# Kernel tuning notes

Measured on AMD Instinct MI355X. Metric: run time of the kernel, lower is better.

## Reference

```python
import jax, jax.numpy as jnp
import numpy as np
from jax import lax

THRESHOLD = 0.8
EPS = 1e-3


def _conv2d_same(x, w, b):
    # x: [B,H,W,Cin], w: [3,3,Cin,Cout], b: [Cout]
    y = lax.conv_general_dilated(x, w, window_strides=(1, 1), padding='SAME',
                                 dimension_numbers=('NHWC', 'HWIO', 'NHWC'))
    return y + b


def _region_moments(x, flag):
    # x: [B,H,W,C], flag: [B,H,W,1] in {0,1}
    flag_sum = jnp.sum(jnp.sign(flag), axis=(1, 2), keepdims=True) + EPS
    mu = jnp.sum(x * flag, axis=(1, 2), keepdims=True) / flag_sum
    sigma = jnp.sum((x - mu) ** 2 * flag, axis=(1, 2), keepdims=True) / flag_sum
    return mu, sigma


def setup_inputs() -> dict:
    key = jax.random.key(0)
    k = jax.random.split(key, 4)
    B, H, W, C = 8, 256, 256, 128
    inputs = jax.random.normal(k[0], (B, H, W, C), dtype=jnp.float32)
    w_sr = jax.random.normal(k[1], (3, 3, 2, 1), dtype=jnp.float32) * 0.3
    w_gamma = jax.random.normal(k[2], (3, 3, 1, 1), dtype=jnp.float32) * 0.3
    w_beta = jax.random.normal(k[3], (3, 3, 1, 1), dtype=jnp.float32) * 0.3
    return {
        'inputs': inputs,
        'w_sr': w_sr, 'b_sr': jnp.zeros((1,), jnp.float32),
        'w_gamma': w_gamma, 'b_gamma': jnp.zeros((1,), jnp.float32),
        'w_beta': w_beta, 'b_beta': jnp.zeros((1,), jnp.float32),
    }


def reference(inputs, w_sr, b_sr, w_gamma, b_gamma, w_beta, b_beta):
    maxpool = jnp.max(inputs, axis=-1, keepdims=True)
    avgpool = jnp.mean(inputs, axis=-1, keepdims=True)
    x = jnp.concatenate([maxpool, avgpool], axis=-1)  # [B,H,W,2]
    x = jax.nn.sigmoid(_conv2d_same(x, w_sr, b_sr))   # [B,H,W,1]
    region_mask = jnp.sign(jax.nn.relu(x - THRESHOLD))  # {0,1}

    beta = _conv2d_same(x, w_beta, b_beta)
    gamma = _conv2d_same(x, w_gamma, b_gamma)

    mu_v, sig_v = _region_moments(inputs, region_mask)
    x_valid = (inputs - mu_v) / jnp.sqrt(sig_v + EPS) * region_mask

    inv_mask = 1.0 - region_mask
    mu_m, sig_m = _region_moments(inputs, inv_mask)
    x_mask = (inputs - mu_m) / jnp.sqrt(sig_m + EPS) * inv_mask

    out = x_valid + x_mask
    return out * beta + gamma
```

## Files before the change

kernel.cpp:

```cpp
#include <hip/hip_runtime.h>

#define BB 8
#define HH 256
#define WW 256
#define CC 128
#define HW (HH*WW)
#define NP (BB*HW)
#define THRESHOLD 0.8f
#define EPSV 1e-3f

__global__ __launch_bounds__(256) void k_pool(const float* __restrict__ in,
                                              float2* __restrict__ pooled,
                                              float* __restrict__ zbuf) {
    if (blockIdx.x == 0) {
        for (int i = threadIdx.x; i < 4104; i += 256) zbuf[i] = 0.0f;
    }
    int p    = blockIdx.x * 4 + (threadIdx.x >> 6);
    int lane = threadIdx.x & 63;
    const float2 v = *reinterpret_cast<const float2*>(in + (size_t)p * CC + lane * 2);
    float mx = fmaxf(v.x, v.y);
    float sm = v.x + v.y;
#pragma unroll
    for (int m = 32; m >= 1; m >>= 1) {
        mx = fmaxf(mx, __shfl_xor(mx, m));
        sm += __shfl_xor(sm, m);
    }
    if (lane == 0) pooled[p] = make_float2(mx, sm * (1.0f / 128.0f));
}

__global__ __launch_bounds__(256) void k_mask(const float2* __restrict__ pooled,
                                              const float* __restrict__ w_sr,
                                              const float* __restrict__ b_sr,
                                              const float* __restrict__ w_gamma,
                                              const float* __restrict__ b_gamma,
                                              const float* __restrict__ w_beta,
                                              const float* __restrict__ b_beta,
                                              float* __restrict__ mask,
                                              float2* __restrict__ bg,
                                              float* __restrict__ cnt) {
    int b    = blockIdx.x >> 6;
    int tile = blockIdx.x & 63;
    int th0  = (tile >> 3) * 32;
    int tw0  = (tile & 7) * 32;
    __shared__ float xs[34][35];
    __shared__ float csh;
    if (threadIdx.x == 0) csh = 0.0f;

    float wsr[18], wg[9], wb[9];
#pragma unroll
    for (int i = 0; i < 18; ++i) wsr[i] = w_sr[i];
#pragma unroll
    for (int i = 0; i < 9; ++i) { wg[i] = w_gamma[i]; wb[i] = w_beta[i]; }
    float bsr = b_sr[0], bg0 = b_gamma[0], bb0 = b_beta[0];

    for (int i = threadIdx.x; i < 34 * 34; i += 256) {
        int ly = i / 34, lx = i - ly * 34;
        int h = th0 + ly - 1, w = tw0 + lx - 1;
        float val = 0.0f;
        if ((unsigned)h < HH && (unsigned)w < WW) {
            float acc = bsr;
#pragma unroll
            for (int kh = 0; kh < 3; ++kh) {
                int hh = h + kh - 1;
                if ((unsigned)hh >= HH) continue;
#pragma unroll
                for (int kw = 0; kw < 3; ++kw) {
                    int ww = w + kw - 1;
                    if ((unsigned)ww >= WW) continue;
                    float2 pv = pooled[(size_t)b * HW + hh * WW + ww];
                    acc += pv.x * wsr[(kh * 3 + kw) * 2 + 0] + pv.y * wsr[(kh * 3 + kw) * 2 + 1];
                }
            }
            val = 1.0f / (1.0f + expf(-acc));
        }
        xs[ly][lx] = val;
    }
    __syncthreads();

    float csum = 0.0f;
    for (int i = threadIdx.x; i < 1024; i += 256) {
        int ty = i >> 5, tx = i & 31;
        float xc = xs[ty + 1][tx + 1];
        float m = (xc > THRESHOLD) ? 1.0f : 0.0f;
        csum += m;
        float ag = bg0, ab = bb0;
#pragma unroll
        for (int kh = 0; kh < 3; ++kh)
#pragma unroll
            for (int kw = 0; kw < 3; ++kw) {
                float xv = xs[ty + kh][tx + kw];
                ag += xv * wg[kh * 3 + kw];
                ab += xv * wb[kh * 3 + kw];
            }
        size_t p = (size_t)b * HW + (size_t)(th0 + ty) * WW + (tw0 + tx);
        mask[p] = m;
        bg[p] = make_float2(ab, ag);
    }
    atomicAdd(&csh, csum);
    __syncthreads();
    if (threadIdx.x == 0) atomicAdd(&cnt[b], csh);
}

__global__ __launch_bounds__(256) void k_moments(const float* __restrict__ in,
                                                 const float* __restrict__ mask,
                                                 float* __restrict__ acc) {
    int b     = blockIdx.x >> 7;
    int chunk = blockIdx.x & 127;
    int c4    = threadIdx.x & 31;
    int pg    = threadIdx.x >> 5;
    float4 sv = make_float4(0, 0, 0, 0), ssv = sv, sm = sv, ssm = sv;
    int pbase = chunk * 512;
    for (int i = 0; i < 64; ++i) {
        int pl = pbase + i * 8 + pg;
        size_t p = (size_t)b * HW + pl;
        float m = mask[p];
        const float4 v = *reinterpret_cast<const float4*>(in + p * CC + c4 * 4);
        float4 v2 = make_float4(v.x * v.x, v.y * v.y, v.z * v.z, v.w * v.w);
        if (m > 0.5f) {
            sv.x += v.x; sv.y += v.y; sv.z += v.z; sv.w += v.w;
            ssv.x += v2.x; ssv.y += v2.y; ssv.z += v2.z; ssv.w += v2.w;
        } else {
            sm.x += v.x; sm.y += v.y; sm.z += v.z; sm.w += v.w;
            ssm.x += v2.x; ssm.y += v2.y; ssm.z += v2.z; ssm.w += v2.w;
        }
    }
    __shared__ float4 sh[4][8][32];
    sh[0][pg][c4] = sv; sh[1][pg][c4] = ssv; sh[2][pg][c4] = sm; sh[3][pg][c4] = ssm;
    __syncthreads();
    int t = threadIdx.x;
    if (t < 128) {
        int arr = t >> 5, c = t & 31;
        float4 s = sh[arr][0][c];
#pragma unroll
        for (int j = 1; j < 8; ++j) {
            float4 u = sh[arr][j][c];
            s.x += u.x; s.y += u.y; s.z += u.z; s.w += u.w;
        }
        float* dst = acc + arr * 1024 + b * 128 + c * 4;
        atomicAdd(dst + 0, s.x);
        atomicAdd(dst + 1, s.y);
        atomicAdd(dst + 2, s.z);
        atomicAdd(dst + 3, s.w);
    }
}

__global__ void k_stats(const float* __restrict__ acc, const float* __restrict__ cnt,
                        float* __restrict__ stats) {
    int i = blockIdx.x * 256 + threadIdx.x;
    if (i >= 1024) return;
    int b = i >> 7;
    float cv = cnt[b];
    float cm = (float)HW - cv;
    float s_v = acc[i], ss_v = acc[1024 + i], s_m = acc[2048 + i], ss_m = acc[3072 + i];
    float fs_v = cv + EPSV;
    float mu_v = s_v / fs_v;
    float sig_v = (ss_v - 2.f * mu_v * s_v + mu_v * mu_v * cv) / fs_v;
    float fs_m = cm + EPSV;
    float mu_m = s_m / fs_m;
    float sig_m = (ss_m - 2.f * mu_m * s_m + mu_m * mu_m * cm) / fs_m;
    stats[i]        = mu_v;
    stats[1024 + i] = 1.0f / sqrtf(sig_v + EPSV);
    stats[2048 + i] = mu_m;
    stats[3072 + i] = 1.0f / sqrtf(sig_m + EPSV);
}

__global__ __launch_bounds__(256) void k_apply(const float* __restrict__ in,
                                               const float* __restrict__ mask,
                                               const float2* __restrict__ bg,
                                               const float* __restrict__ stats,
                                               float* __restrict__ out) {
    size_t idx = (size_t)blockIdx.x * 256 + threadIdx.x;
    size_t p = idx >> 5;
    int c4 = (int)(idx & 31);
    int b = (int)(p >> 16);
    const float4 v = reinterpret_cast<const float4*>(in)[idx];
    float m   = mask[p];
    float2 bgv = bg[p];
    float be = bgv.x, ga = bgv.y;
    int off = (m > 0.5f) ? 0 : 2048;
    int si = off + b * 128 + c4 * 4;
    const float4 mu = *reinterpret_cast<const float4*>(stats + si);
    const float4 rs = *reinterpret_cast<const float4*>(stats + si + 1024);
    float4 o;
    o.x = (v.x - mu.x) * rs.x * be + ga;
    o.y = (v.y - mu.y) * rs.y * be + ga;
    o.z = (v.z - mu.z) * rs.z * be + ga;
    o.w = (v.w - mu.w) * rs.w * be + ga;
    reinterpret_cast<float4*>(out)[idx] = o;
}

extern "C" void kernel_launch(void* const* d_in, const int* in_sizes, int n_in,
                              void* d_out, int out_size, void* d_ws, size_t ws_size,
                              hipStream_t stream) {
    const float* in      = (const float*)d_in[0];
    const float* w_sr    = (const float*)d_in[1];
    const float* b_sr    = (const float*)d_in[2];
    const float* w_gamma = (const float*)d_in[3];
    const float* b_gamma = (const float*)d_in[4];
    const float* w_beta  = (const float*)d_in[5];
    const float* b_beta  = (const float*)d_in[6];
    float* out = (float*)d_out;
    float* ws  = (float*)d_ws;

    float2* pooled = (float2*)ws;
    float*  mask   = ws + 2 * (size_t)NP;
    float2* bg     = (float2*)(ws + 3 * (size_t)NP);
    float*  acc    = ws + 5 * (size_t)NP;
    float*  cnt    = acc + 4096;
    float*  stats  = cnt + 8;

    k_pool   <<<NP / 4,  256, 0, stream>>>(in, pooled, acc);
    k_mask   <<<BB * 64, 256, 0, stream>>>(pooled, w_sr, b_sr, w_gamma, b_gamma,
                                           w_beta, b_beta, mask, bg, cnt);
    k_moments<<<BB * 128, 256, 0, stream>>>(in, mask, acc);
    k_stats  <<<4, 256, 0, stream>>>(acc, cnt, stats);
    k_apply  <<<(int)((size_t)NP * CC / 4 / 256), 256, 0, stream>>>(in, mask, bg, stats, out);
}
```

Measured before the change: 580.8 us.

## Fuse total moments into pooling pass and accumulate only minority mask region

New measurement: 552.3 us. -4.9%, faster.

```diff
diff --git a/kernel.cpp b/kernel.cpp
--- a/kernel.cpp
+++ b/kernel.cpp
@@ -11,21 +11,49 @@
 
 __global__ __launch_bounds__(256) void k_pool(const float* __restrict__ in,
                                               float2* __restrict__ pooled,
-                                              float* __restrict__ zbuf) {
-    if (blockIdx.x == 0) {
-        for (int i = threadIdx.x; i < 4104; i += 256) zbuf[i] = 0.0f;
-    }
-    int p    = blockIdx.x * 4 + (threadIdx.x >> 6);
-    int lane = threadIdx.x & 63;
-    const float2 v = *reinterpret_cast<const float2*>(in + (size_t)p * CC + lane * 2);
-    float mx = fmaxf(v.x, v.y);
-    float sm = v.x + v.y;
-#pragma unroll
-    for (int m = 32; m >= 1; m >>= 1) {
-        mx = fmaxf(mx, __shfl_xor(mx, m));
-        sm += __shfl_xor(sm, m);
-    }
-    if (lane == 0) pooled[p] = make_float2(mx, sm * (1.0f / 128.0f));
+                                              float* __restrict__ accT,
+                                              float* __restrict__ accTS) {
+    int b     = blockIdx.x >> 7;
+    int chunk = blockIdx.x & 127;
+    int c4    = threadIdx.x & 31;
+    int pg    = threadIdx.x >> 5;
+    int base  = chunk * 512;
+    float4 tT  = make_float4(0, 0, 0, 0), tTS = tT;
+    for (int i = 0; i < 64; ++i) {
+        int pl = base + i * 8 + pg;
+        size_t p = (size_t)b * HW + pl;
+        const float4 v = *reinterpret_cast<const float4*>(in + p * CC + c4 * 4);
+        tT.x += v.x; tT.y += v.y; tT.z += v.z; tT.w += v.w;
+        tTS.x += v.x * v.x; tTS.y += v.y * v.y; tTS.z += v.z * v.z; tTS.w += v.w * v.w;
+        float mx = fmaxf(fmaxf(v.x, v.y), fmaxf(v.z, v.w));
+        float sm = v.x + v.y + v.z + v.w;
+#pragma unroll
+        for (int msk = 16; msk >= 1; msk >>= 1) {
+            mx = fmaxf(mx, __shfl_xor(mx, msk));
+            sm += __shfl_xor(sm, msk);
+        }
+        if (c4 == 0) pooled[p] = make_float2(mx, sm * (1.0f / 128.0f));
+    }
+    __shared__ float4 shT[8][32];
+    __shared__ float4 shS[8][32];
+    shT[pg][c4] = tT;
+    shS[pg][c4] = tTS;
+    __syncthreads();
+    int t = threadIdx.x;
+    if (t < 64) {
+        int arr = t >> 5, c = t & 31;
+        float4 s = arr ? shS[0][c] : shT[0][c];
+#pragma unroll
+        for (int j = 1; j < 8; ++j) {
+            float4 u = arr ? shS[j][c] : shT[j][c];
+            s.x += u.x; s.y += u.y; s.z += u.z; s.w += u.w;
+        }
+        float* dst = (arr ? accTS : accT) + b * 128 + c * 4;
+        atomicAdd(dst + 0, s.x);
+        atomicAdd(dst + 1, s.y);
+        atomicAdd(dst + 2, s.z);
+        atomicAdd(dst + 3, s.w);
+    }
 }
 
 __global__ __launch_bounds__(256) void k_mask(const float2* __restrict__ pooled,
@@ -103,40 +131,41 @@
 
 __global__ __launch_bounds__(256) void k_moments(const float* __restrict__ in,
                                                  const float* __restrict__ mask,
-                                                 float* __restrict__ acc) {
+                                                 const float* __restrict__ cnt,
+                                                 float* __restrict__ accV,
+                                                 float* __restrict__ accVS) {
     int b     = blockIdx.x >> 7;
     int chunk = blockIdx.x & 127;
     int c4    = threadIdx.x & 31;
     int pg    = threadIdx.x >> 5;
-    float4 sv = make_float4(0, 0, 0, 0), ssv = sv, sm = sv, ssm = sv;
+    bool tgt1 = cnt[b] <= (float)(HW / 2);
+    float4 sv = make_float4(0, 0, 0, 0), ssv = sv;
     int pbase = chunk * 512;
     for (int i = 0; i < 64; ++i) {
         int pl = pbase + i * 8 + pg;
         size_t p = (size_t)b * HW + pl;
-        float m = mask[p];
-        const float4 v = *reinterpret_cast<const float4*>(in + p * CC + c4 * 4);
-        float4 v2 = make_float4(v.x * v.x, v.y * v.y, v.z * v.z, v.w * v.w);
-        if (m > 0.5f) {
+        bool mv = mask[p] > 0.5f;
+        if (mv == tgt1) {
+            const float4 v = *reinterpret_cast<const float4*>(in + p * CC + c4 * 4);
             sv.x += v.x; sv.y += v.y; sv.z += v.z; sv.w += v.w;
-            ssv.x += v2.x; ssv.y += v2.y; ssv.z += v2.z; ssv.w += v2.w;
-        } else {
-            sm.x += v.x; sm.y += v.y; sm.z += v.z; sm.w += v.w;
-            ssm.x += v2.x; ssm.y += v2.y; ssm.z += v2.z; ssm.w += v2.w;
-        }
-    }
-    __shared__ float4 sh[4][8][32];
-    sh[0][pg][c4] = sv; sh[1][pg][c4] = ssv; sh[2][pg][c4] = sm; sh[3][pg][c4] = ssm;
+            ssv.x += v.x * v.x; ssv.y += v.y * v.y; ssv.z += v.z * v.z; ssv.w += v.w * v.w;
+        }
+    }
+    __shared__ float4 shV[8][32];
+    __shared__ float4 shS[8][32];
+    shV[pg][c4] = sv;
+    shS[pg][c4] = ssv;
     __syncthreads();
     int t = threadIdx.x;
-    if (t < 128) {
+    if (t < 64) {
         int arr = t >> 5, c = t & 31;
-        float4 s = sh[arr][0][c];
+        float4 s = arr ? shS[0][c] : shV[0][c];
 #pragma unroll
         for (int j = 1; j < 8; ++j) {
-            float4 u = sh[arr][j][c];
+            float4 u = arr ? shS[j][c] : shV[j][c];
             s.x += u.x; s.y += u.y; s.z += u.z; s.w += u.w;
         }
-        float* dst = acc + arr * 1024 + b * 128 + c * 4;
+        float* dst = (arr ? accVS : accV) + b * 128 + c * 4;
         atomicAdd(dst + 0, s.x);
         atomicAdd(dst + 1, s.y);
         atomicAdd(dst + 2, s.z);
@@ -144,14 +173,19 @@
     }
 }
 
-__global__ void k_stats(const float* __restrict__ acc, const float* __restrict__ cnt,
-                        float* __restrict__ stats) {
+__global__ void k_stats(const float* __restrict__ accT, const float* __restrict__ accTS,
+                        const float* __restrict__ accV, const float* __restrict__ accVS,
+                        const float* __restrict__ cnt, float* __restrict__ stats) {
     int i = blockIdx.x * 256 + threadIdx.x;
     if (i >= 1024) return;
     int b = i >> 7;
     float cv = cnt[b];
     float cm = (float)HW - cv;
-    float s_v = acc[i], ss_v = acc[1024 + i], s_m = acc[2048 + i], ss_m = acc[3072 + i];
+    bool tgt1 = cv <= (float)(HW / 2);
+    float T = accT[i], TS = accTS[i], s_t = accV[i], ss_t = accVS[i];
+    float s_v, ss_v, s_m, ss_m;
+    if (tgt1) { s_v = s_t; ss_v = ss_t; s_m = T - s_t; ss_m = TS - ss_t; }
+    else      { s_m = s_t; ss_m = ss_t; s_v = T - s_t; ss_v = TS - ss_t; }
     float fs_v = cv + EPSV;
     float mu_v = s_v / fs_v;
     float sig_v = (ss_v - 2.f * mu_v * s_v + mu_v * mu_v * cv) / fs_v;
@@ -174,7 +208,7 @@
     int c4 = (int)(idx & 31);
     int b = (int)(p >> 16);
     const float4 v = reinterpret_cast<const float4*>(in)[idx];
-    float m   = mask[p];
+    float m    = mask[p];
     float2 bgv = bg[p];
     float be = bgv.x, ga = bgv.y;
     int off = (m > 0.5f) ? 0 : 2048;
@@ -205,14 +239,19 @@
     float2* pooled = (float2*)ws;
     float*  mask   = ws + 2 * (size_t)NP;
     float2* bg     = (float2*)(ws + 3 * (size_t)NP);
-    float*  acc    = ws + 5 * (size_t)NP;
-    float*  cnt    = acc + 4096;
+    float*  accT   = ws + 5 * (size_t)NP;
+    float*  accTS  = accT + 1024;
+    float*  accV   = accTS + 1024;
+    float*  accVS  = accV + 1024;
+    float*  cnt    = accVS + 1024;
     float*  stats  = cnt + 8;
 
-    k_pool   <<<NP / 4,  256, 0, stream>>>(in, pooled, acc);
+    hipMemsetAsync(accT, 0, (4096 + 8) * sizeof(float), stream);
+
+    k_pool   <<<BB * 128, 256, 0, stream>>>(in, pooled, accT, accTS);
     k_mask   <<<BB * 64, 256, 0, stream>>>(pooled, w_sr, b_sr, w_gamma, b_gamma,
                                            w_beta, b_beta, mask, bg, cnt);
-    k_moments<<<BB * 128, 256, 0, stream>>>(in, mask, acc);
-    k_stats  <<<4, 256, 0, stream>>>(acc, cnt, stats);
+    k_moments<<<BB * 128, 256, 0, stream>>>(in, mask, cnt, accV, accVS);
+    k_stats  <<<4, 256, 0, stream>>>(accT, accTS, accV, accVS, cnt, stats);
     k_apply  <<<(int)((size_t)NP * CC / 4 / 256), 256, 0, stream>>>(in, mask, bg, stats, out);
 }
```
